# Optimization experiments

Hardware: AMD Instinct MI355X
Metric: run time of the kernel (lower is better)

## Reference

```python
import jax, jax.numpy as jnp
import numpy as np

HIDDEN = 2048
NUM_HEADS = 16
HEAD_DIM = 128
INNER = NUM_HEADS * HEAD_DIM
ROPE_BASE = 10000.0


def apply_rope(x):
    # x: [B, H, S, D], rotate-half (NeoX-style) RoPE
    B, H, S, D = x.shape
    inv_freq = 1.0 / (ROPE_BASE ** (jnp.arange(0, D, 2, dtype=jnp.float32) / D))
    t = jnp.arange(S, dtype=jnp.float32)
    freqs = t[:, None] * inv_freq[None, :]          # [S, D/2]
    cos = jnp.concatenate([jnp.cos(freqs)] * 2, -1)  # [S, D]
    sin = jnp.concatenate([jnp.sin(freqs)] * 2, -1)
    x1, x2 = x[..., : D // 2], x[..., D // 2:]
    rotated = jnp.concatenate([-x2, x1], axis=-1)
    return x * cos[None, None] + rotated * sin[None, None]


def setup_inputs() -> dict:
    key = jax.random.key(0)
    ks = jax.random.split(key, 9)
    s = 1.0 / np.sqrt(HIDDEN)
    return {
        "hidden_states": jax.random.normal(ks[0], (2, 2048, HIDDEN), jnp.float32),
        "Wq": jax.random.uniform(ks[1], (INNER, HIDDEN), jnp.float32, -s, s),
        "bq": jax.random.uniform(ks[2], (INNER,), jnp.float32, -s, s),
        "Wk": jax.random.uniform(ks[3], (INNER, HIDDEN), jnp.float32, -s, s),
        "bk": jax.random.uniform(ks[4], (INNER,), jnp.float32, -s, s),
        "Wv": jax.random.uniform(ks[5], (INNER, HIDDEN), jnp.float32, -s, s),
        "bv": jax.random.uniform(ks[6], (INNER,), jnp.float32, -s, s),
        "Wo": jax.random.uniform(ks[7], (HIDDEN, INNER), jnp.float32, -s, s),
        "bo": jax.random.uniform(ks[8], (HIDDEN,), jnp.float32, -s, s),
    }


def reference(hidden_states, Wq, bq, Wk, bk, Wv, bv, Wo, bo):
    B, S, _ = hidden_states.shape

    def heads(x):  # [B,S,inner] -> [B,H,S,D]
        return x.reshape(B, S, NUM_HEADS, HEAD_DIM).transpose(0, 2, 1, 3)

    q = heads(hidden_states @ Wq.T + bq)
    k = heads(hidden_states @ Wk.T + bk)
    v = heads(hidden_states @ Wv.T + bv)
    q = apply_rope(q)
    k = apply_rope(k)

    scores = jnp.einsum("bhqd,bhkd->bhqk", q, k) / jnp.sqrt(
        jnp.asarray(HEAD_DIM, q.dtype))
    causal = jnp.tril(jnp.ones((S, S), dtype=bool))
    scores = jnp.where(causal[None, None], scores, jnp.finfo(scores.dtype).min)
    weights = jax.nn.softmax(scores, axis=-1)
    context = jnp.einsum("bhqk,bhkd->bhqd", weights, v)
    merged = context.transpose(0, 2, 1, 3).reshape(B, S, INNER)
    return merged @ Wo.T + bo
```

## Files before the change

### kernel.cpp

```cpp
#include <hip/hip_runtime.h>

using u16 = unsigned short;
using u32 = unsigned int;

typedef __attribute__((ext_vector_type(4))) float f32x4;
typedef __attribute__((ext_vector_type(8))) short frag8;

#define HIDDEN 2048
#define SEQ    2048
#define NHEADS 16
#define HDIM   128

__device__ __forceinline__ float bf2f(u16 u) {
  union { u32 i; float f; } c; c.i = ((u32)u) << 16; return c.f;
}
__device__ __forceinline__ u16 f2bf(float f) {
  union { float f; u32 i; } c; c.f = f;
  u32 u = c.i + 0x7fffu + ((c.i >> 16) & 1u);
  return (u16)(u >> 16);
}

__global__ void cvt_all(const float* __restrict__ X,
                        const float* __restrict__ W0, const float* __restrict__ W1,
                        const float* __restrict__ W2, const float* __restrict__ W3,
                        u16* __restrict__ dX,
                        u16* __restrict__ dW0, u16* __restrict__ dW1,
                        u16* __restrict__ dW2, u16* __restrict__ dW3)
{
  const int bx = blockIdx.x;
  const float* s; u16* d; int g;
  if (bx < 4096) { s = X; d = dX; g = bx * 256 + threadIdx.x; }
  else {
    const int t = bx - 4096;
    const int w = t >> 11;
    s = (w == 0) ? W0 : (w == 1) ? W1 : (w == 2) ? W2 : W3;
    d = (w == 0) ? dW0 : (w == 1) ? dW1 : (w == 2) ? dW2 : dW3;
    g = (t & 2047) * 256 + threadIdx.x;
  }
  const float* p = s + (size_t)g * 8;
  f32x4 x0 = *(const f32x4*)p, x1 = *(const f32x4*)(p + 4);
  frag8 o;
#pragma unroll
  for (int e = 0; e < 4; e++) { o[e] = (short)f2bf(x0[e]); o[e+4] = (short)f2bf(x1[e]); }
  *(frag8*)(d + (size_t)g * 8) = o;
}

template<int W_BF16, int NW, int VT, int C_F32>
__global__ __launch_bounds__(256, 4)
void gemm_fused(const u16* __restrict__ A,
                const void* __restrict__ W0, const void* __restrict__ W1,
                const void* __restrict__ W2,
                const float* __restrict__ bias0, const float* __restrict__ bias1,
                const float* __restrict__ bias2,
                void* __restrict__ C0, void* __restrict__ C1, void* __restrict__ C2)
{
  __shared__ __align__(16) u16 smem[8192];
  u16* As = smem;
  u16* Bs = smem + 4096;

  const int tid  = threadIdx.x;
  const int lane = tid & 63;
  const int wv   = tid >> 6;
  const int quad = lane >> 4;
  const int l16  = lane & 15;
  const int wm = wv >> 1, wn = wv & 1;
  const int m0 = blockIdx.y * 128;
  const int wix = (NW == 1) ? 0 : (blockIdx.x >> 4);
  const int n0  = ((NW == 1) ? blockIdx.x : (blockIdx.x & 15)) * 128;

  const void* Wp = (wix == 0) ? W0 : (wix == 1) ? W1 : W2;
  const float* bias = (wix == 0) ? bias0 : (wix == 1) ? bias1 : bias2;
  void* Cp = (wix == 0) ? C0 : (wix == 1) ? C1 : C2;

  f32x4 acc[4][4];
#pragma unroll
  for (int i = 0; i < 4; i++)
#pragma unroll
    for (int j = 0; j < 4; j++) acc[i][j] = (f32x4)0.0f;

  const int g0 = tid, g1 = tid + 256;
  const int r0 = g0 >> 2, c0 = (g0 & 3) * 8;
  const int r1 = g1 >> 2, c1 = (g1 & 3) * 8;

  for (int k0 = 0; k0 < HIDDEN; k0 += 32) {
    __builtin_amdgcn_global_load_lds(
      (const __attribute__((address_space(1))) void*)(A + (size_t)(m0 + r0) * HIDDEN + k0 + c0),
      (__attribute__((address_space(3))) void*)(As + g0 * 8), 16, 0, 0);
    __builtin_amdgcn_global_load_lds(
      (const __attribute__((address_space(1))) void*)(A + (size_t)(m0 + r1) * HIDDEN + k0 + c1),
      (__attribute__((address_space(3))) void*)(As + g1 * 8), 16, 0, 0);
    if (W_BF16) {
      const u16* Wb = (const u16*)Wp;
      __builtin_amdgcn_global_load_lds(
        (const __attribute__((address_space(1))) void*)(Wb + (size_t)(n0 + r0) * HIDDEN + k0 + c0),
        (__attribute__((address_space(3))) void*)(Bs + g0 * 8), 16, 0, 0);
      __builtin_amdgcn_global_load_lds(
        (const __attribute__((address_space(1))) void*)(Wb + (size_t)(n0 + r1) * HIDDEN + k0 + c1),
        (__attribute__((address_space(3))) void*)(Bs + g1 * 8), 16, 0, 0);
    } else {
      const float* Wf = (const float*)Wp;
      const float* p0 = Wf + (size_t)(n0 + r0) * HIDDEN + k0 + c0;
      const float* p1 = Wf + (size_t)(n0 + r1) * HIDDEN + k0 + c1;
      f32x4 x0 = *(const f32x4*)p0, x1 = *(const f32x4*)(p0 + 4);
      f32x4 y0 = *(const f32x4*)p1, y1 = *(const f32x4*)(p1 + 4);
      frag8 b0v, b1v;
#pragma unroll
      for (int e = 0; e < 4; e++) {
        b0v[e]   = (short)f2bf(x0[e]); b0v[e+4] = (short)f2bf(x1[e]);
        b1v[e]   = (short)f2bf(y0[e]); b1v[e+4] = (short)f2bf(y1[e]);
      }
      *(frag8*)&Bs[g0 * 8] = b0v;
      *(frag8*)&Bs[g1 * 8] = b1v;
    }

    __builtin_amdgcn_s_waitcnt(0);
    __syncthreads();

    frag8 af[4], bfr[4];
#pragma unroll
    for (int mt = 0; mt < 4; mt++)
      af[mt] = *(const frag8*)&As[(wm*64 + mt*16 + l16) * 32 + quad*8];
#pragma unroll
    for (int nt = 0; nt < 4; nt++)
      bfr[nt] = *(const frag8*)&Bs[(wn*64 + nt*16 + l16) * 32 + quad*8];
#pragma unroll
    for (int mt = 0; mt < 4; mt++)
#pragma unroll
      for (int nt = 0; nt < 4; nt++)
        acc[mt][nt] = __builtin_amdgcn_mfma_f32_16x16x32_bf16(af[mt], bfr[nt], acc[mt][nt], 0, 0, 0);

    __syncthreads();
  }

  if (VT && wix == 2) {
    u16* Cv = (u16*)Cp;
    u16* T = smem + wv * 1056;
#pragma unroll
    for (int nt = 0; nt < 4; nt++) {
      const int n  = n0 + wn*64 + nt*16 + l16;
      const float bv = bias[n];
#pragma unroll
      for (int mt = 0; mt < 4; mt++)
#pragma unroll
        for (int r = 0; r < 4; r++)
          T[l16 * 66 + mt*16 + quad*4 + r] = f2bf(acc[mt][nt][r] + bv);
#pragma unroll
      for (int rr = 0; rr < 16; rr++) {
        const int nn = n0 + wn*64 + nt*16 + rr;
        const int mm = m0 + wm*64 + lane;
        const int b = mm >> 11, s = mm & 2047;
        Cv[((size_t)(b * HIDDEN + nn)) * SEQ + s] = T[rr * 66 + lane];
      }
    }
  } else {
#pragma unroll
    for (int nt = 0; nt < 4; nt++) {
      const int n  = n0 + wn*64 + nt*16 + l16;
      const float bv = bias[n];
#pragma unroll
      for (int mt = 0; mt < 4; mt++) {
#pragma unroll
        for (int r = 0; r < 4; r++) {
          const int m = m0 + wm*64 + mt*16 + quad*4 + r;
          if (C_F32) ((float*)Cp)[(size_t)m * HIDDEN + n] = acc[mt][nt][r] + bv;
          else       ((u16*)Cp)[(size_t)m * HIDDEN + n]   = f2bf(acc[mt][nt][r] + bv);
        }
      }
    }
  }
}

#define NT32 32

#define STG(gptr, lofs) __builtin_amdgcn_global_load_lds( \
    (const __attribute__((address_space(1))) void*)(gptr), \
    (__attribute__((address_space(3))) void*)(smem + (lofs)), 16, 0, 0)

#define GRP(t, DOSTAGE, WAITSTR) { \
  u16* As = smem + ((t) % 3) * 24576; \
  u16* Bs = As + 16384; \
  if (DOSTAGE) { \
    const size_t ko = (size_t)((t)+2)*64; const int sb = (((t)+2)%3)*24576; \
    STG(gA0 + ko, sb + ldsA0); STG(gA1 + ko, sb + ldsA1); STG(gB0 + ko, sb + ldsB0); \
    STG(gA2 + ko, sb + ldsA2); STG(gA3 + ko, sb + ldsA3); STG(gB1 + ko, sb + ldsB1); \
  } \
  frag8 af0[4], bf0[4], af1[4], bf1[4]; \
  _Pragma("unroll") for (int mt = 0; mt < 4; mt++) \
    af0[mt] = *(const frag8*)(As + abase + mt*1024 + s0q); \
  _Pragma("unroll") for (int nt = 0; nt < 4; nt++) \
    bf0[nt] = *(const frag8*)(Bs + bbase + nt*1024 + s0q); \
  _Pragma("unroll") for (int mt = 0; mt < 4; mt++) \
    af1[mt] = *(const frag8*)(As + abase + mt*1024 + s1q); \
  _Pragma("unroll") for (int nt = 0; nt < 4; nt++) \
    bf1[nt] = *(const frag8*)(Bs + bbase + nt*1024 + s1q); \
  asm volatile("s_waitcnt lgkmcnt(0) " WAITSTR ::: "memory"); \
  __builtin_amdgcn_s_barrier(); \
  __builtin_amdgcn_s_setprio(1); \
  _Pragma("unroll") for (int mt = 0; mt < 4; mt++) \
    _Pragma("unroll") for (int nt = 0; nt < 4; nt++) \
      acc[mt][nt] = __builtin_amdgcn_mfma_f32_16x16x32_bf16(af0[mt], bf0[nt], acc[mt][nt], 0,0,0); \
  _Pragma("unroll") for (int mt = 0; mt < 4; mt++) \
    _Pragma("unroll") for (int nt = 0; nt < 4; nt++) \
      acc[mt][nt] = __builtin_amdgcn_mfma_f32_16x16x32_bf16(af1[mt], bf1[nt], acc[mt][nt], 0,0,0); \
  __builtin_amdgcn_s_setprio(0); \
}

#define G256_SETUP(Abase, Wbase) \
  const int tid  = threadIdx.x; \
  const int lane = tid & 63; \
  const int wv   = tid >> 6; \
  const int quad = lane >> 4; \
  const int l16  = lane & 15; \
  const int wm = wv >> 1, wn = wv & 1; \
  const int c8 = (lane & 7) ^ (lane >> 3); \
  const int rA = lane >> 3; \
  const u16* gA0 = (Abase) + (size_t)(m0 + wv*32 +  0 + rA) * HIDDEN + c8*8; \
  const u16* gA1 = (Abase) + (size_t)(m0 + wv*32 +  8 + rA) * HIDDEN + c8*8; \
  const u16* gA2 = (Abase) + (size_t)(m0 + wv*32 + 16 + rA) * HIDDEN + c8*8; \
  const u16* gA3 = (Abase) + (size_t)(m0 + wv*32 + 24 + rA) * HIDDEN + c8*8; \
  const u16* gB0 = (Wbase) + (size_t)(n0 + wv*16 +  0 + rA) * HIDDEN + c8*8; \
  const u16* gB1 = (Wbase) + (size_t)(n0 + wv*16 +  8 + rA) * HIDDEN + c8*8; \
  const int ldsA0 = (4*wv)*512 + lane*8; \
  const int ldsA1 = ldsA0 + 512; \
  const int ldsA2 = ldsA0 + 1024; \
  const int ldsA3 = ldsA0 + 1536; \
  const int ldsB0 = 16384 + (2*wv)*512 + lane*8; \
  const int ldsB1 = ldsB0 + 512; \
  const int s0q = ((quad    ) ^ (l16 & 7)) * 8; \
  const int s1q = ((quad + 4) ^ (l16 & 7)) * 8; \
  const int abase = (wm*64 + l16) * 64; \
  const int bbase = (wn*64 + l16) * 64; \
  f32x4 acc[4][4]; \
  _Pragma("unroll") \
  for (int i = 0; i < 4; i++) \
    _Pragma("unroll") \
    for (int j = 0; j < 4; j++) acc[i][j] = (f32x4)0.0f; \
  STG(gA0, ldsA0); STG(gA1, ldsA1); STG(gB0, ldsB0); \
  STG(gA2, ldsA2); STG(gA3, ldsA3); STG(gB1, ldsB1); \
  STG(gA0 + 64, 24576 + ldsA0); STG(gA1 + 64, 24576 + ldsA1); STG(gB0 + 64, 24576 + ldsB0); \
  STG(gA2 + 64, 24576 + ldsA2); STG(gA3 + 64, 24576 + ldsA3); STG(gB1 + 64, 24576 + ldsB1); \
  asm volatile("s_waitcnt vmcnt(6)" ::: "memory"); \
  __builtin_amdgcn_s_barrier(); \
  for (int t = 0; t < NT32 - 2; ++t) GRP(t, 1, "vmcnt(6)"); \
  GRP(NT32 - 2, 0, "vmcnt(0)"); \
  GRP(NT32 - 1, 0, "vmcnt(63)"); \
  __syncthreads();

__global__ __launch_bounds__(512, 1)
void gemm256_qkv(const u16* __restrict__ A,
                 const u16* __restrict__ W0, const u16* __restrict__ W1,
                 const u16* __restrict__ W2,
                 const float* __restrict__ bias0, const float* __restrict__ bias1,
                 const float* __restrict__ bias2,
                 u16* __restrict__ C0, u16* __restrict__ C1, u16* __restrict__ Vt)
{
  __shared__ __align__(16) u16 smem[73728];

  const int bid = blockIdx.x;
  const int sbid = (bid & 7) * 96 + (bid >> 3);
  const int colTile = sbid >> 4;
  const int rowTile = sbid & 15;
  const int wix = colTile >> 4;
  const int n0  = (colTile & 15) * 128;
  const int m0  = rowTile * 256;

  const u16* Wp = (wix == 0) ? W0 : (wix == 1) ? W1 : W2;
  const float* bias = (wix == 0) ? bias0 : (wix == 1) ? bias1 : bias2;

  G256_SETUP(A, Wp)

  if (wix != 2) {
    const float scale = (wix == 0) ? 0.08838834764831845f : 1.0f;
    u16* T = smem;
#pragma unroll
    for (int nt = 0; nt < 4; nt++) {
      const int nl = wn*64 + nt*16 + l16;
      const float bv = bias[n0 + nl];
#pragma unroll
      for (int mt = 0; mt < 4; mt++) {
        const int ml = wm*64 + mt*16 + quad*4;
#pragma unroll
        for (int r = 0; r < 4; r++)
          T[(ml + r)*128 + nl] = f2bf((acc[mt][nt][r] + bv) * scale);
      }
    }
    __syncthreads();

    u16* Cb = (wix == 0) ? C0 : C1;
    const int mr = tid >> 1, qd = tid & 1;
    const float s = (float)((m0 + mr) & 2047);
#pragma unroll
    for (int c8i = 0; c8i < 4; c8i++) {
      const int d0 = qd*32 + c8i*8;
      frag8 lo = *(const frag8*)&T[mr*128 + d0];
      frag8 hi = *(const frag8*)&T[mr*128 + 64 + d0];
      frag8 olo, ohi;
#pragma unroll
      for (int e = 0; e < 8; e++) {
        const float inv = __expf(-(float)(d0 + e) * (9.210340371976184f / 64.0f));
        float sn, c;
        __sincosf(s * inv, &sn, &c);
        const float x1 = bf2f((u16)lo[e]), x2 = bf2f((u16)hi[e]);
        olo[e] = (short)f2bf(x1 * c - x2 * sn);
        ohi[e] = (short)f2bf(x2 * c + x1 * sn);
      }
      *(frag8*)&Cb[(size_t)(m0 + mr) * HIDDEN + n0 + d0]      = olo;
      *(frag8*)&Cb[(size_t)(m0 + mr) * HIDDEN + n0 + 64 + d0] = ohi;
    }
  } else {
    u16* T = smem + wv * 1152;
    const int b  = m0 >> 11;
    const int s0 = (m0 & 2047) + wm*64;
#pragma unroll
    for (int nt = 0; nt < 4; nt++) {
      const int nloc = n0 + wn*64 + nt*16;
      const float bv = bias[nloc + l16];
#pragma unroll
      for (int mt = 0; mt < 4; mt++)
#pragma unroll
        for (int r = 0; r < 4; r++)
          T[l16*72 + mt*16 + quad*4 + r] = f2bf(acc[mt][nt][r] + bv);
#pragma unroll
      for (int rr = 0; rr < 16; rr++) {
        const size_t vb = ((size_t)(b * HIDDEN + nloc + rr)) * SEQ + s0;
        Vt[vb + lane] = T[rr*72 + lane];
      }
    }
  }
}

__global__ __launch_bounds__(512, 1)
void gemm256_o(const u16* __restrict__ A, const u16* __restrict__ W,
               const float* __restrict__ bias, float* __restrict__ C)
{
  __shared__ __align__(16) u16 smem[73728];

  const int bid = blockIdx.x;
  const int sbid = (bid & 7) * 32 + (bid >> 3);
  const int colTile = sbid >> 4;
  const int rowTile = sbid & 15;
  const int n0  = colTile * 128;
  const int m0  = rowTile * 256;

  G256_SETUP(A, W)

#pragma unroll
  for (int nt = 0; nt < 4; nt++) {
    const int n = n0 + wn*64 + nt*16 + l16;
    const float bv = bias[n];
#pragma unroll
    for (int mt = 0; mt < 4; mt++) {
      const int m = m0 + wm*64 + mt*16 + quad*4;
#pragma unroll
      for (int r = 0; r < 4; r++)
        C[(size_t)(m + r) * HIDDEN + n] = acc[mt][nt][r] + bv;
    }
  }
}

__global__ void rope_kernel(u16* __restrict__ Q, u16* __restrict__ K)
{
  const int tid = blockIdx.x * 256 + threadIdx.x;
  const int t   = tid >> 19;
  const int r   = tid & 524287;
  const int row = r >> 7;
  const int grp = r & 127;
  const int h   = grp >> 3, d0 = (grp & 7) * 8;
  u16* X = t ? K : Q;
  const float s = (float)(row & 2047);
  const float qscale = t ? 1.0f : 0.08838834764831845f;
  const size_t base = (size_t)row * HIDDEN + h * HDIM + d0;
  frag8 a = *(const frag8*)(X + base);
  frag8 b = *(const frag8*)(X + base + 64);
  frag8 oa, ob;
#pragma unroll
  for (int e = 0; e < 8; e++) {
    const float inv = __expf(-(float)(d0 + e) * (9.210340371976184f / 64.0f));
    float sn, c;
    __sincosf(s * inv, &sn, &c);
    const float x1 = bf2f((u16)a[e]), x2 = bf2f((u16)b[e]);
    oa[e] = (short)f2bf((x1 * c - x2 * sn) * qscale);
    ob[e] = (short)f2bf((x2 * c + x1 * sn) * qscale);
  }
  *(frag8*)(X + base)      = oa;
  *(frag8*)(X + base + 64) = ob;
}

__global__ __launch_bounds__(256, 3)
void attn_kernel(const u16* Q, const u16* __restrict__ K,
                 const u16* __restrict__ Vt, u16* O)
{
  __shared__ __align__(16) u16 smem[20480];

  const int bx = blockIdx.x;
  const int g  = bx >> 5;
  const int bh = bx & 31;
  const int qt = (g & 1) ? (31 - (g >> 1)) : (g >> 1);
  const int b = bh >> 4, h = bh & 15;

  const int tid = threadIdx.x, lane = tid & 63, wv = tid >> 6;
  const int quad = lane >> 4, l16 = lane & 15;
  const int l7 = l16 & 7;

  const size_t krow0 = (size_t)(b * SEQ) * HIDDEN + h * HDIM;
  const size_t vrow0 = (size_t)(b * HIDDEN + h * HDIM) * SEQ;

  frag8 qf[4];
  const size_t qbase = ((size_t)(b * SEQ) + qt*64 + wv*16) * HIDDEN + h * HDIM;
#pragma unroll
  for (int ks = 0; ks < 4; ks++)
    qf[ks] = *(const frag8*)(Q + qbase + (size_t)l16 * HIDDEN + ks*32 + quad*8);

  const int kr4 = lane >> 4, kc = lane & 15;
  const int vr8 = lane >> 3;
  const u16* gK[4]; const u16* gV[4];
  int ldsK[4], ldsV[4];
#pragma unroll
  for (int it = 0; it < 4; it++) {
    const int kcs = kc ^ ((it*4 + kr4) & 7);
    gK[it] = K + krow0 + (size_t)(wv*16 + it*4 + kr4) * HIDDEN + kcs*8;
    ldsK[it] = (wv*16 + it*4)*128 + lane*8;
    const int vcs = (lane & 7) ^ vr8;
    gV[it] = Vt + vrow0 + (size_t)(wv*32 + it*8 + vr8) * SEQ + vcs*8;
    ldsV[it] = 8192 + (wv*32 + it*8)*64 + lane*8;
  }

  f32x4 Oacc[8];
#pragma unroll
  for (int dt = 0; dt < 8; dt++) Oacc[dt] = (f32x4)0.0f;
  float m_i[4], l_i[4];
#pragma unroll
  for (int r = 0; r < 4; r++) { m_i[r] = -1e30f; l_i[r] = 0.0f; }

  const int ktmax = qt + 1;
  u16* Pw = smem + 16384 + wv*1024;

  for (int kt = 0; kt < ktmax; kt++) {
#pragma unroll
    for (int it = 0; it < 4; it++) {
      __builtin_amdgcn_global_load_lds(
        (const __attribute__((address_space(1))) void*)(gK[it] + (size_t)kt*64*HIDDEN),
        (__attribute__((address_space(3))) void*)(smem + ldsK[it]), 16, 0, 0);
      __builtin_amdgcn_global_load_lds(
        (const __attribute__((address_space(1))) void*)(gV[it] + kt*64),
        (__attribute__((address_space(3))) void*)(smem + ldsV[it]), 16, 0, 0);
    }
    asm volatile("s_waitcnt vmcnt(0)" ::: "memory");
    __syncthreads();

    f32x4 st[4];
#pragma unroll
    for (int jt = 0; jt < 4; jt++) st[jt] = (f32x4)0.0f;

    __builtin_amdgcn_s_setprio(1);
#pragma unroll
    for (int ks = 0; ks < 4; ks++) {
      frag8 kf[4];
#pragma unroll
      for (int jt = 0; jt < 4; jt++)
        kf[jt] = *(const frag8*)&smem[(jt*16 + l16)*128 + ((ks*4 + quad) ^ l7)*8];
#pragma unroll
      for (int jt = 0; jt < 4; jt++)
        st[jt] = __builtin_amdgcn_mfma_f32_16x16x32_bf16(qf[ks], kf[jt], st[jt], 0, 0, 0);
    }
    __builtin_amdgcn_s_setprio(0);

    if (kt == qt) {
#pragma unroll
      for (int jt = 0; jt < 4; jt++) {
        const int jl = jt*16 + l16;
#pragma unroll
        for (int r = 0; r < 4; r++) {
          const int ml = wv*16 + quad*4 + r;
          st[jt][r] = (jl <= ml) ? st[jt][r] : -1e30f;
        }
      }
    }

    float alpha[4];
    int needresc = 0;
#pragma unroll
    for (int r = 0; r < 4; r++) {
      float cm = fmaxf(fmaxf(st[0][r], st[1][r]), fmaxf(st[2][r], st[3][r]));
      cm = fmaxf(cm, __shfl_xor(cm, 1, 64));
      cm = fmaxf(cm, __shfl_xor(cm, 2, 64));
      cm = fmaxf(cm, __shfl_xor(cm, 4, 64));
      cm = fmaxf(cm, __shfl_xor(cm, 8, 64));
      if (cm > m_i[r] + 8.0f) {
        alpha[r] = __expf(m_i[r] - cm);
        m_i[r] = cm;
        needresc = 1;
      } else {
        alpha[r] = 1.0f;
      }
    }

    float csum[4];
#pragma unroll
    for (int r = 0; r < 4; r++) csum[r] = 0.0f;
#pragma unroll
    for (int jt = 0; jt < 4; jt++)
#pragma unroll
      for (int r = 0; r < 4; r++) {
        const float p = __expf(st[jt][r] - m_i[r]);
        csum[r] += p;
        const int prow = quad*4 + r;
        Pw[prow*64 + (((jt*2 + (l16 >> 3)) ^ (prow & 7)) << 3) + l7] = f2bf(p);
      }
#pragma unroll
    for (int r = 0; r < 4; r++) {
      float cs = csum[r];
      cs += __shfl_xor(cs, 1, 64);
      cs += __shfl_xor(cs, 2, 64);
      cs += __shfl_xor(cs, 4, 64);
      cs += __shfl_xor(cs, 8, 64);
      l_i[r] = l_i[r] * alpha[r] + cs;
    }
    if (__any(needresc)) {
#pragma unroll
      for (int r = 0; r < 4; r++)
#pragma unroll
        for (int dt = 0; dt < 8; dt++) Oacc[dt][r] *= alpha[r];
    }

    __builtin_amdgcn_s_setprio(1);
#pragma unroll
    for (int ks2 = 0; ks2 < 2; ks2++) {
      frag8 pf = *(const frag8*)&Pw[l16*64 + ((ks2*4 + quad) ^ l7)*8];
#pragma unroll
      for (int dt = 0; dt < 8; dt++) {
        frag8 vf = *(const frag8*)&smem[8192 + (dt*16 + l16)*64 + ((ks2*4 + quad) ^ l7)*8];
        Oacc[dt] = __builtin_amdgcn_mfma_f32_16x16x32_bf16(pf, vf, Oacc[dt], 0, 0, 0);
      }
    }
    __builtin_amdgcn_s_setprio(0);
    __syncthreads();
  }

#pragma unroll
  for (int r = 0; r < 4; r++) {
    const float inv = 1.0f / l_i[r];
    const int m = qt*64 + wv*16 + quad*4 + r;
#pragma unroll
    for (int dt = 0; dt < 8; dt++) {
      const int d = dt*16 + l16;
      O[((size_t)(b * SEQ) + m) * HIDDEN + h * HDIM + d] = f2bf(Oacc[dt][r] * inv);
    }
  }
}

extern "C" void kernel_launch(void* const* d_in, const int* in_sizes, int n_in,
                              void* d_out, int out_size, void* d_ws, size_t ws_size,
                              hipStream_t stream)
{
  const float* X  = (const float*)d_in[0];
  const float* Wq = (const float*)d_in[1];
  const float* bq = (const float*)d_in[2];
  const float* Wk = (const float*)d_in[3];
  const float* bk = (const float*)d_in[4];
  const float* Wv = (const float*)d_in[5];
  const float* bv = (const float*)d_in[6];
  const float* Wo = (const float*)d_in[7];
  const float* bo = (const float*)d_in[8];
  float* out = (float*)d_out;

  u16* Kb = (u16*)d_out;
  u16* Xb = (u16*)d_out + (8u << 20);
  char* ws = (char*)d_ws;
  u16* Qb  = (u16*)ws;
  u16* Vtb = (u16*)(ws + (16u << 20));

  dim3 blk(256);
  const bool fast = ws_size >= (64u << 20);
  if (fast) {
    u16* Wqb = (u16*)(ws + (32u << 20));
    u16* Wkb = (u16*)(ws + (40u << 20));
    u16* Wvb = (u16*)(ws + (48u << 20));
    u16* Wob = (u16*)(ws + (56u << 20));
    cvt_all<<<12288, blk, 0, stream>>>(X, Wq, Wk, Wv, Wo, Xb, Wqb, Wkb, Wvb, Wob);
    gemm256_qkv<<<dim3(768), dim3(512), 0, stream>>>(
        Xb, Wqb, Wkb, Wvb, bq, bk, bv, Qb, Kb, Vtb);
    attn_kernel<<<1024, blk, 0, stream>>>(Qb, Kb, Vtb, Qb);
    gemm256_o<<<dim3(256), dim3(512), 0, stream>>>(Qb, Wob, bo, out);
  } else {
    cvt_all<<<4096, blk, 0, stream>>>(X, Wq, Wk, Wv, Wo, Xb, Xb, Xb, Xb, Xb);
    gemm_fused<0,3,1,0><<<dim3(48,32), blk, 0, stream>>>(
        Xb, Wq, Wk, Wv, bq, bk, bv, Qb, Kb, Vtb);
    rope_kernel<<<4096, blk, 0, stream>>>(Qb, Kb);
    attn_kernel<<<1024, blk, 0, stream>>>(Qb, Kb, Vtb, Qb);
    gemm_fused<0,1,0,1><<<dim3(16,32), blk, 0, stream>>>(
        Qb, Wo, Wo, Wo, bo, bo, bo, out, out, out);
  }
}
```

Measured before the change: 400.7 us.

## Double-buffer LDS fragment registers to overlap reads with MFMA in GEMM mainloop

Restructures the bf16 GEMM main loop so fragments for the next k-tile are read from LDS into a second register set while MFMAs run on the current set, ping-ponging between X and Y fragment arrays. Previously each iteration read all fragments, waited on lgkmcnt(0), then issued MFMAs, which serialised LDS latency with compute. The new schedule adds an extra barrier per half-step and doubles fragment register use, which raises VGPR pressure at 512 threads per block.

```diff
diff --git a/kernel.cpp b/kernel.cpp
--- a/kernel.cpp
+++ b/kernel.cpp
@@ -176,32 +176,33 @@
     (const __attribute__((address_space(1))) void*)(gptr), \
     (__attribute__((address_space(3))) void*)(smem + (lofs)), 16, 0, 0)
 
-#define GRP(t, DOSTAGE, WAITSTR) { \
-  u16* As = smem + ((t) % 3) * 24576; \
-  u16* Bs = As + 16384; \
-  if (DOSTAGE) { \
-    const size_t ko = (size_t)((t)+2)*64; const int sb = (((t)+2)%3)*24576; \
-    STG(gA0 + ko, sb + ldsA0); STG(gA1 + ko, sb + ldsA1); STG(gB0 + ko, sb + ldsB0); \
-    STG(gA2 + ko, sb + ldsA2); STG(gA3 + ko, sb + ldsA3); STG(gB1 + ko, sb + ldsB1); \
-  } \
-  frag8 af0[4], bf0[4], af1[4], bf1[4]; \
+#define STAGE6(ti) { \
+  const size_t ko_ = (size_t)(ti)*64; const int sb_ = ((ti)%3)*24576; \
+  STG(gA0 + ko_, sb_ + ldsA0); STG(gA1 + ko_, sb_ + ldsA1); STG(gB0 + ko_, sb_ + ldsB0); \
+  STG(gA2 + ko_, sb_ + ldsA2); STG(gA3 + ko_, sb_ + ldsA3); STG(gB1 + ko_, sb_ + ldsB1); \
+}
+
+#define READF(F, ti) { \
+  u16* As_ = smem + ((ti) % 3) * 24576; \
+  u16* Bs_ = As_ + 16384; \
   _Pragma("unroll") for (int mt = 0; mt < 4; mt++) \
-    af0[mt] = *(const frag8*)(As + abase + mt*1024 + s0q); \
+    F##a0[mt] = *(const frag8*)(As_ + abase + mt*1024 + s0q); \
   _Pragma("unroll") for (int nt = 0; nt < 4; nt++) \
-    bf0[nt] = *(const frag8*)(Bs + bbase + nt*1024 + s0q); \
+    F##b0[nt] = *(const frag8*)(Bs_ + bbase + nt*1024 + s0q); \
   _Pragma("unroll") for (int mt = 0; mt < 4; mt++) \
-    af1[mt] = *(const frag8*)(As + abase + mt*1024 + s1q); \
+    F##a1[mt] = *(const frag8*)(As_ + abase + mt*1024 + s1q); \
   _Pragma("unroll") for (int nt = 0; nt < 4; nt++) \
-    bf1[nt] = *(const frag8*)(Bs + bbase + nt*1024 + s1q); \
-  asm volatile("s_waitcnt lgkmcnt(0) " WAITSTR ::: "memory"); \
-  __builtin_amdgcn_s_barrier(); \
+    F##b1[nt] = *(const frag8*)(Bs_ + bbase + nt*1024 + s1q); \
+}
+
+#define MFMAF(F) { \
   __builtin_amdgcn_s_setprio(1); \
   _Pragma("unroll") for (int mt = 0; mt < 4; mt++) \
     _Pragma("unroll") for (int nt = 0; nt < 4; nt++) \
-      acc[mt][nt] = __builtin_amdgcn_mfma_f32_16x16x32_bf16(af0[mt], bf0[nt], acc[mt][nt], 0,0,0); \
+      acc[mt][nt] = __builtin_amdgcn_mfma_f32_16x16x32_bf16(F##a0[mt], F##b0[nt], acc[mt][nt], 0,0,0); \
   _Pragma("unroll") for (int mt = 0; mt < 4; mt++) \
     _Pragma("unroll") for (int nt = 0; nt < 4; nt++) \
-      acc[mt][nt] = __builtin_amdgcn_mfma_f32_16x16x32_bf16(af1[mt], bf1[nt], acc[mt][nt], 0,0,0); \
+      acc[mt][nt] = __builtin_amdgcn_mfma_f32_16x16x32_bf16(F##a1[mt], F##b1[nt], acc[mt][nt], 0,0,0); \
   __builtin_amdgcn_s_setprio(0); \
 }
 
@@ -235,15 +236,28 @@
   for (int i = 0; i < 4; i++) \
     _Pragma("unroll") \
     for (int j = 0; j < 4; j++) acc[i][j] = (f32x4)0.0f; \
-  STG(gA0, ldsA0); STG(gA1, ldsA1); STG(gB0, ldsB0); \
-  STG(gA2, ldsA2); STG(gA3, ldsA3); STG(gB1, ldsB1); \
-  STG(gA0 + 64, 24576 + ldsA0); STG(gA1 + 64, 24576 + ldsA1); STG(gB0 + 64, 24576 + ldsB0); \
-  STG(gA2 + 64, 24576 + ldsA2); STG(gA3 + 64, 24576 + ldsA3); STG(gB1 + 64, 24576 + ldsB1); \
+  frag8 Xa0[4], Xb0[4], Xa1[4], Xb1[4]; \
+  frag8 Ya0[4], Yb0[4], Ya1[4], Yb1[4]; \
+  STAGE6(0) STAGE6(1) \
   asm volatile("s_waitcnt vmcnt(6)" ::: "memory"); \
   __builtin_amdgcn_s_barrier(); \
-  for (int t = 0; t < NT32 - 2; ++t) GRP(t, 1, "vmcnt(6)"); \
-  GRP(NT32 - 2, 0, "vmcnt(0)"); \
-  GRP(NT32 - 1, 0, "vmcnt(63)"); \
+  READF(X, 0) \
+  for (int t = 0; t < NT32; t += 2) { \
+     \
+    if (t + 2 < NT32) { STAGE6(t+2) asm volatile("s_waitcnt vmcnt(6)" ::: "memory"); } \
+    else              { asm volatile("s_waitcnt vmcnt(0)" ::: "memory"); } \
+    __builtin_amdgcn_s_barrier(); \
+    READF(Y, t+1) \
+    MFMAF(X) \
+    __builtin_amdgcn_s_barrier(); \
+     \
+    if (t + 3 < NT32)      { STAGE6(t+3) asm volatile("s_waitcnt vmcnt(6)" ::: "memory"); } \
+    else if (t + 2 < NT32) { asm volatile("s_waitcnt vmcnt(0)" ::: "memory"); } \
+    __builtin_amdgcn_s_barrier(); \
+    if (t + 2 < NT32) READF(X, t+2) \
+    MFMAF(Y) \
+    __builtin_amdgcn_s_barrier(); \
+  } \
   __syncthreads();
 
 __global__ __launch_bounds__(512, 1)
```

After: 408.4 us. About the same (+1.9%).
